# Kernel tuning notes

Hardware: AMD Instinct MI355X
Metric: run time of the kernel (lower is better)

Reference implementation:

```python
import jax, jax.numpy as jnp
import numpy as np

NUM_EXPERTS = 3
SCALING = 8.0 / 8.0  # alpha / r


def setup_inputs() -> dict:
    key = jax.random.key(0)
    ks = jax.random.split(key, 8)
    B, H, W, D = 64, 28, 28, 512
    Dh = 4 * D
    E, K, R = 3, 2, 8
    T = B * H * W
    x = jax.random.normal(ks[0], (B, H, W, D), dtype=jnp.float32)
    W1 = jax.random.normal(ks[1], (D, Dh), dtype=jnp.float32) * (1.0 / D ** 0.5)
    b1 = jnp.zeros((Dh,), dtype=jnp.float32)
    W2 = jax.random.normal(ks[2], (Dh, D), dtype=jnp.float32) * (1.0 / Dh ** 0.5)
    b2 = jnp.zeros((D,), dtype=jnp.float32)
    w_down = jax.random.normal(ks[3], (E, D, R), dtype=jnp.float32) * (1.0 / D ** 0.5)
    # original init is zeros; use small randn so output/grads are non-trivial
    w_up = jax.random.normal(ks[4], (E, R, D), dtype=jnp.float32) * 0.02
    gate_logits = jax.random.normal(ks[5], (T, E), dtype=jnp.float32)
    gate_probs = jax.nn.softmax(gate_logits, axis=-1)
    topk_probs, topk_indices = jax.lax.top_k(gate_probs, K)
    topk_indices = topk_indices.astype(jnp.int64)
    return {"x": x, "W1": W1, "b1": b1, "W2": W2, "b2": b2,
            "w_down": w_down, "w_up": w_up, "gate_probs": gate_probs,
            "topk_probs": topk_probs, "topk_indices": topk_indices}


def reference(x, W1, b1, W2, b2, w_down, w_up, gate_probs, topk_probs, topk_indices):
    # frozen base ConvNeXt MLP (channels-last): Linear -> GELU -> Linear
    orig_out = jax.nn.gelu(jnp.dot(x, W1) + b1, approximate=False) @ W2 + b2

    D = x.shape[-1]
    x_flat = x.reshape(-1, D)  # [T, D]

    # dense per-expert LoRA over all tokens (rank-8, cheap), then mask-combine
    down = jnp.einsum('td,edr->etr', x_flat, w_down)          # [E, T, r]
    up = jnp.einsum('etr,erd->etd', jax.nn.gelu(down, approximate=False), w_up) * SCALING  # [E, T, D]

    # weights[e, t] = sum_k topk_probs[t, k] * (topk_indices[t, k] == e)
    E = w_down.shape[0]
    mask = (topk_indices[None, :, :] == jnp.arange(E)[:, None, None])  # [E, T, K]
    weights = jnp.sum(jnp.where(mask, topk_probs[None], 0.0), axis=-1)  # [E, T]

    moe_out = jnp.einsum('et,etd->td', weights, up).reshape(x.shape)
    return orig_out + moe_out
```

## Files before the change

kernel.cpp:

```cpp
#include <hip/hip_runtime.h>

typedef _Float16 f16;
typedef _Float16 f16x8 __attribute__((ext_vector_type(8)));
typedef _Float16 f16x4 __attribute__((ext_vector_type(4)));
typedef float f32x4 __attribute__((ext_vector_type(4)));

#define TD 512
#define TDH 2048

__device__ __forceinline__ float gelu_fast(float x) {
  float u = x * fmaf(x * x, 0.0713548162f, 1.595769122f);
  float e = __expf(-u);
  return x * __builtin_amdgcn_rcpf(1.0f + e);
}

__device__ __forceinline__ void glds16(const f16* g, f16* l) {
  __builtin_amdgcn_global_load_lds(
      (const __attribute__((address_space(1))) void*)g,
      (__attribute__((address_space(3))) void*)l, 16, 0, 0);
}

__global__ __launch_bounds__(256) void k_conv_x(f16* __restrict__ dst,
                                                const float* __restrict__ src,
                                                int n4) {
  int i = blockIdx.x * 256 + threadIdx.x;
  if (i >= n4) return;
  float4 v = ((const float4*)src)[i];
  f16x4 o = {(f16)v.x, (f16)v.y, (f16)v.z, (f16)v.w};
  ((f16x4*)dst)[i] = o;
}

__global__ void k_trans(f16* __restrict__ dst, const float* __restrict__ src,
                        int R, int C) {
  __shared__ float t[32][33];
  const int bx = blockIdx.x, by = blockIdx.y;
  const int tx = threadIdx.x, ty = threadIdx.y;
#pragma unroll
  for (int s = 0; s < 32; s += 8)
    t[ty + s][tx] = src[(size_t)(by * 32 + ty + s) * C + bx * 32 + tx];
  __syncthreads();
#pragma unroll
  for (int s = 0; s < 32; s += 8)
    dst[(size_t)(bx * 32 + ty + s) * R + by * 32 + tx] = (f16)t[tx][ty + s];
}

__global__ __launch_bounds__(256) void k_wdT(f16* __restrict__ dst,
                                             const float* __restrict__ wd) {
  int i = blockIdx.x * 256 + threadIdx.x;
  int n = i >> 9, k = i & 511;
  float v = (n < 24) ? wd[(size_t)((n >> 3) * 512 + k) * 8 + (n & 7)] : 0.0f;
  dst[i] = (f16)v;
}

__global__ __launch_bounds__(256) void k_wuT(f16* __restrict__ dst,
                                             const float* __restrict__ wu) {
  int i = blockIdx.x * 256 + threadIdx.x;
  int d = i >> 5, er = i & 31;
  float v = (er < 24) ? wu[(size_t)(er >> 3) * 4096 + (er & 7) * 512 + d] : 0.0f;
  dst[i] = (f16)v;
}

template <int EPI, int NBN>
__global__ __launch_bounds__(256) void k_gemm(
    const f16* __restrict__ A, const f16* __restrict__ B, int Kt, int lda,
    int ldb, const float* __restrict__ bias, f16* __restrict__ Hout, int ldh,
    float* __restrict__ Out, int ldc, const float* __restrict__ tkp,
    const int* __restrict__ tki, const f16* __restrict__ Ag,
    const f16* __restrict__ Bg) {
  __shared__ __align__(16) f16 As[2][128 * 32];
  __shared__ __align__(16) f16 Bs[2][128 * 32];
  const int tid = threadIdx.x;
  const int lane = tid & 63;
  const int w = tid >> 6;
  const int wm = w >> 1, wn = w & 1;

  const int nwg = gridDim.x;
  const int q = nwg >> 3, r = nwg & 7;
  const int xcd = blockIdx.x & 7, pos = blockIdx.x >> 3;
  const int swz =
      (xcd < r ? xcd * (q + 1) : r * (q + 1) + (xcd - r) * q) + pos;
  const int bm = swz / NBN, bn = swz % NBN;

  const int c0 = 2 * w;
  const int lrow = lane >> 2;
  const int srow = c0 * 16 + lrow;
  const int skk = ((lane & 3) ^ ((lrow >> 1) & 3)) * 8;
  const f16* gA = A + (size_t)(bm * 128 + srow) * lda + skk;
  const f16* gB = B + (size_t)(bn * 128 + srow) * ldb + skk;
  f16* lA0 = &As[0][c0 * 512];
  f16* lA1 = &As[1][c0 * 512];
  f16* lB0 = &Bs[0][c0 * 512];
  f16* lB1 = &Bs[1][c0 * 512];

  f32x4 acc[4][4] = {};
  const int frow = lane & 15;
  const int swk = ((lane >> 4) ^ ((frow >> 1) & 3)) * 8;
  const int nt = Kt / 32;

  glds16(gA, lA0);
  glds16(gA + (size_t)16 * lda, lA0 + 512);
  glds16(gB, lB0);
  glds16(gB + (size_t)16 * ldb, lB0 + 512);
  __syncthreads();

  for (int t = 0; t < nt; ++t) {
    f16* dA = (t & 1) ? lA0 : lA1;
    f16* dB = (t & 1) ? lB0 : lB1;
    if (t + 1 < nt) {
      const int k = (t + 1) * 32;
      glds16(gA + k, dA);
      glds16(gA + k + (size_t)16 * lda, dA + 512);
      glds16(gB + k, dB);
      glds16(gB + k + (size_t)16 * ldb, dB + 512);
    } else if (EPI == 1) {
      const f16* gAg = Ag + (size_t)(bm * 128 + srow) * 32 + skk;
      const f16* gBg = Bg + (size_t)(bn * 128 + srow) * 32 + skk;
      glds16(gAg, dA);
      glds16(gAg + 512, dA + 512);
      glds16(gBg, dB);
      glds16(gBg + 512, dB + 512);
    }
    const f16* rA = As[t & 1];
    const f16* rB = Bs[t & 1];
    f16x8 af[4], bf[4];
#pragma unroll
    for (int i = 0; i < 4; i++)
      af[i] = *(const f16x8*)&rA[(wm * 64 + i * 16 + frow) * 32 + swk];
#pragma unroll
    for (int j = 0; j < 4; j++)
      bf[j] = *(const f16x8*)&rB[(wn * 64 + j * 16 + frow) * 32 + swk];
#pragma unroll
    for (int i = 0; i < 4; i++)
#pragma unroll
      for (int j = 0; j < 4; j++)
        acc[i][j] = __builtin_amdgcn_mfma_f32_16x16x32_f16(bf[j], af[i],
                                                           acc[i][j], 0, 0, 0);
    __syncthreads();
  }

  if constexpr (EPI == 1) {
    const f16* rA = As[nt & 1];
    const f16* rB = Bs[nt & 1];
    f16x8 af[4], bf[4];
#pragma unroll
    for (int i = 0; i < 4; i++)
      af[i] = *(const f16x8*)&rA[(wm * 64 + i * 16 + frow) * 32 + swk];
#pragma unroll
    for (int j = 0; j < 4; j++)
      bf[j] = *(const f16x8*)&rB[(wn * 64 + j * 16 + frow) * 32 + swk];
#pragma unroll
    for (int i = 0; i < 4; i++)
#pragma unroll
      for (int j = 0; j < 4; j++)
        acc[i][j] = __builtin_amdgcn_mfma_f32_16x16x32_f16(bf[j], af[i],
                                                           acc[i][j], 0, 0, 0);
  }

  const int m0 = wm * 64 + (lane & 15);
  const int n0 = wn * 64 + ((lane >> 4) << 2);

  if constexpr (EPI == 0) {
#pragma unroll
    for (int i = 0; i < 4; i++) {
      const size_t rb = (size_t)(bm * 128 + m0 + i * 16) * ldh + bn * 128 + n0;
#pragma unroll
      for (int j = 0; j < 4; j++) {
        const float4 bb = *(const float4*)&bias[bn * 128 + n0 + j * 16];
        f16x4 o = {(f16)gelu_fast(acc[i][j][0] + bb.x),
                   (f16)gelu_fast(acc[i][j][1] + bb.y),
                   (f16)gelu_fast(acc[i][j][2] + bb.z),
                   (f16)gelu_fast(acc[i][j][3] + bb.w)};
        *(f16x4*)&Hout[rb + j * 16] = o;
      }
    }
  } else if constexpr (EPI == 1) {
#pragma unroll
    for (int i = 0; i < 4; i++) {
      const size_t rb = (size_t)(bm * 128 + m0 + i * 16) * ldc + bn * 128 + n0;
#pragma unroll
      for (int j = 0; j < 4; j++) {
        const float4 bb = *(const float4*)&bias[bn * 128 + n0 + j * 16];
        float4 v = {acc[i][j][0] + bb.x, acc[i][j][1] + bb.y,
                    acc[i][j][2] + bb.z, acc[i][j][3] + bb.w};
        *(float4*)&Out[rb + j * 16] = v;
      }
    }
  } else {
    if (wn == 0) {
#pragma unroll
      for (int i = 0; i < 4; i++) {
        const int m = bm * 128 + m0 + i * 16;
        const int i0 = tki[m * 2], i1 = tki[m * 2 + 1];
        const float p0 = tkp[m * 2], p1 = tkp[m * 2 + 1];
#pragma unroll
        for (int j = 0; j < 2; j++) {
          const int nb = n0 + j * 16;
          const int e = nb >> 3;
          const float wgt = (i0 == e ? p0 : 0.0f) + (i1 == e ? p1 : 0.0f);
          f16x4 o = {(f16)(wgt * gelu_fast(acc[i][j][0])),
                     (f16)(wgt * gelu_fast(acc[i][j][1])),
                     (f16)(wgt * gelu_fast(acc[i][j][2])),
                     (f16)(wgt * gelu_fast(acc[i][j][3]))};
          *(f16x4*)&Hout[(size_t)m * 32 + nb] = o;
        }
      }
    }
  }
}

extern "C" void kernel_launch(void* const* d_in, const int* in_sizes, int n_in,
                              void* d_out, int out_size, void* d_ws,
                              size_t ws_size, hipStream_t stream) {
  const float* x = (const float*)d_in[0];
  const float* W1 = (const float*)d_in[1];
  const float* b1 = (const float*)d_in[2];
  const float* W2 = (const float*)d_in[3];
  const float* b2 = (const float*)d_in[4];
  const float* wd = (const float*)d_in[5];
  const float* wu = (const float*)d_in[6];
  const float* tkp = (const float*)d_in[8];
  const int* tki = (const int*)d_in[9];
  float* out = (float*)d_out;

  const int T = in_sizes[0] / TD;

  char* p = (char*)d_ws;
  f16* W1T = (f16*)p; p += (size_t)TDH * TD * sizeof(f16);
  f16* W2T = (f16*)p; p += (size_t)TD * TDH * sizeof(f16);
  f16* wdT = (f16*)p; p += (size_t)128 * TD * sizeof(f16);
  f16* wuT = (f16*)p; p += (size_t)TD * 32 * sizeof(f16);
  size_t fixed = (size_t)(p - (char*)d_ws);
  const size_t per_tok = (size_t)(TD + TDH + 32) * sizeof(f16);
  long mc = (long)((ws_size > fixed ? ws_size - fixed : 0) / per_tok);
  if (mc > T) mc = T;
  mc = (mc / 128) * 128;
  if (mc < 128) mc = 128;
  f16* xb = (f16*)p; p += (size_t)mc * TD * sizeof(f16);
  f16* Hb = (f16*)p; p += (size_t)mc * TDH * sizeof(f16);
  f16* gb = (f16*)p;

  k_trans<<<dim3(TDH / 32, TD / 32), dim3(32, 8), 0, stream>>>(W1T, W1, TD,
                                                               TDH);
  k_trans<<<dim3(TD / 32, TDH / 32), dim3(32, 8), 0, stream>>>(W2T, W2, TDH,
                                                               TD);
  k_wdT<<<dim3(65536 / 256), 256, 0, stream>>>(wdT, wd);
  k_wuT<<<dim3(16384 / 256), 256, 0, stream>>>(wuT, wu);

  for (long off = 0; off < T; off += mc) {
    long m = T - off;
    if (m > mc) m = mc;
    const int mt = (int)(m / 128);
    const int n4 = (int)(m * TD / 4);
    k_conv_x<<<dim3((n4 + 255) / 256), 256, 0, stream>>>(xb, x + off * TD, n4);
    k_gemm<2, 1><<<dim3(mt), 256, 0, stream>>>(
        xb, wdT, TD, TD, TD, nullptr, gb, 32, nullptr, 0, tkp + off * 2,
        tki + off * 2, nullptr, nullptr);
    k_gemm<0, 16><<<dim3(mt * 16), 256, 0, stream>>>(
        xb, W1T, TD, TD, TD, b1, Hb, TDH, nullptr, 0, nullptr, nullptr,
        nullptr, nullptr);
    k_gemm<1, 4><<<dim3(mt * 4), 256, 0, stream>>>(
        Hb, W2T, TDH, TDH, TDH, b2, nullptr, 0, out + off * TD, TD, nullptr,
        nullptr, gb, wuT);
  }
}
```

Before: 567.5 us.

## Widen GEMM K-tile to 64 and fold LoRA down-projection into first GEMM

The GEMM K-step doubles from 32 to 64 with a new XOR swizzle. That halves the number of barrier and loop iterations and issues two MFMAs per fragment pair. The LoRA down-projection is merged into the W1 GEMM as an extra 17th N-block, which removes a separate kernel launch and a second read of x. The gate buffer and up-weights are padded to 64 columns so the LoRA up-projection becomes one extra K-step in the W2 GEMM. The costs are double the LDS use (64KB), possible occupancy loss, and wasted MFMA work on the zero padding.

```diff
diff --git a/kernel.cpp b/kernel.cpp
--- a/kernel.cpp
+++ b/kernel.cpp
@@ -55,20 +55,20 @@
 __global__ __launch_bounds__(256) void k_wuT(f16* __restrict__ dst,
                                              const float* __restrict__ wu) {
   int i = blockIdx.x * 256 + threadIdx.x;
-  int d = i >> 5, er = i & 31;
+  int d = i >> 6, er = i & 63;
   float v = (er < 24) ? wu[(size_t)(er >> 3) * 4096 + (er & 7) * 512 + d] : 0.0f;
   dst[i] = (f16)v;
 }
 
 template <int EPI, int NBN>
-__global__ __launch_bounds__(256) void k_gemm(
-    const f16* __restrict__ A, const f16* __restrict__ B, int Kt, int lda,
-    int ldb, const float* __restrict__ bias, f16* __restrict__ Hout, int ldh,
-    float* __restrict__ Out, int ldc, const float* __restrict__ tkp,
-    const int* __restrict__ tki, const f16* __restrict__ Ag,
-    const f16* __restrict__ Bg) {
-  __shared__ __align__(16) f16 As[2][128 * 32];
-  __shared__ __align__(16) f16 Bs[2][128 * 32];
+__global__ __launch_bounds__(256) void k_gemm64(
+    const f16* __restrict__ A, const f16* __restrict__ B, int NT, int ntm,
+    int lda, int ldb, const float* __restrict__ bias, f16* __restrict__ Hout,
+    int ldh, f16* __restrict__ Gout, float* __restrict__ Out, int ldc,
+    const float* __restrict__ tkp, const int* __restrict__ tki,
+    const f16* __restrict__ Ag, const f16* __restrict__ Bg) {
+  __shared__ __align__(16) f16 As[2][128 * 64];
+  __shared__ __align__(16) f16 Bs[2][128 * 64];
   const int tid = threadIdx.x;
   const int lane = tid & 63;
   const int w = tid >> 6;
@@ -81,99 +81,124 @@
       (xcd < r ? xcd * (q + 1) : r * (q + 1) + (xcd - r) * q) + pos;
   const int bm = swz / NBN, bn = swz % NBN;
 
-  const int c0 = 2 * w;
-  const int lrow = lane >> 2;
-  const int srow = c0 * 16 + lrow;
-  const int skk = ((lane & 3) ^ ((lrow >> 1) & 3)) * 8;
-  const f16* gA = A + (size_t)(bm * 128 + srow) * lda + skk;
-  const f16* gB = B + (size_t)(bn * 128 + srow) * ldb + skk;
-  f16* lA0 = &As[0][c0 * 512];
-  f16* lA1 = &As[1][c0 * 512];
-  f16* lB0 = &Bs[0][c0 * 512];
-  f16* lB1 = &Bs[1][c0 * 512];
+  const int r0 = lane >> 3;
+  const int ssl = (lane & 7) ^ r0;
+  const f16* pA[4];
+  const f16* pB[4];
+  const f16* qA[4];
+  const f16* qB[4];
+#pragma unroll
+  for (int c = 0; c < 4; c++) {
+    const int rg = c * 4 + w;
+    const int row = rg * 8 + r0;
+    pA[c] = A + (size_t)(bm * 128 + row) * lda + ssl * 8;
+    pB[c] = B + (size_t)(bn * 128 + row) * ldb + ssl * 8;
+    if constexpr (EPI == 1) {
+      qA[c] = Ag + (size_t)(bm * 128 + row) * 64 + ssl * 8;
+      qB[c] = Bg + (size_t)(bn * 128 + row) * 64 + ssl * 8;
+    }
+  }
+
+#define STAGE(S, BUF)                                                    \
+  do {                                                                   \
+    if (EPI == 1 && (S) == ntm) {                                        \
+      _Pragma("unroll") for (int c = 0; c < 4; c++) {                    \
+        glds16(qA[c], &As[BUF][(c * 4 + w) * 512]);                      \
+        glds16(qB[c], &Bs[BUF][(c * 4 + w) * 512]);                      \
+      }                                                                  \
+    } else {                                                             \
+      const size_t o = (size_t)(S) * 64;                                 \
+      _Pragma("unroll") for (int c = 0; c < 4; c++) {                    \
+        glds16(pA[c] + o, &As[BUF][(c * 4 + w) * 512]);                  \
+        glds16(pB[c] + o, &Bs[BUF][(c * 4 + w) * 512]);                  \
+      }                                                                  \
+    }                                                                    \
+  } while (0)
 
   f32x4 acc[4][4] = {};
   const int frow = lane & 15;
-  const int swk = ((lane >> 4) ^ ((frow >> 1) & 3)) * 8;
-  const int nt = Kt / 32;
-
-  glds16(gA, lA0);
-  glds16(gA + (size_t)16 * lda, lA0 + 512);
-  glds16(gB, lB0);
-  glds16(gB + (size_t)16 * ldb, lB0 + 512);
+  const int fq = lane >> 4;
+  const int fx = frow & 7;
+  const int sA0 = ((fq ^ fx)) * 8;
+  const int sA1 = (((4 | fq) ^ fx)) * 8;
+  const int aRow = (wm * 64 + frow) * 64;
+  const int bRow = (wn * 64 + frow) * 64;
+
+  STAGE(0, 0);
   __syncthreads();
 
-  for (int t = 0; t < nt; ++t) {
-    f16* dA = (t & 1) ? lA0 : lA1;
-    f16* dB = (t & 1) ? lB0 : lB1;
-    if (t + 1 < nt) {
-      const int k = (t + 1) * 32;
-      glds16(gA + k, dA);
-      glds16(gA + k + (size_t)16 * lda, dA + 512);
-      glds16(gB + k, dB);
-      glds16(gB + k + (size_t)16 * ldb, dB + 512);
-    } else if (EPI == 1) {
-      const f16* gAg = Ag + (size_t)(bm * 128 + srow) * 32 + skk;
-      const f16* gBg = Bg + (size_t)(bn * 128 + srow) * 32 + skk;
-      glds16(gAg, dA);
-      glds16(gAg + 512, dA + 512);
-      glds16(gBg, dB);
-      glds16(gBg + 512, dB + 512);
-    }
+  for (int t = 0; t < NT; ++t) {
+    if (t + 1 < NT) STAGE(t + 1, (t + 1) & 1);
     const f16* rA = As[t & 1];
     const f16* rB = Bs[t & 1];
-    f16x8 af[4], bf[4];
+    f16x8 af[4][2], bf[4][2];
+#pragma unroll
+    for (int i = 0; i < 4; i++) {
+      af[i][0] = *(const f16x8*)&rA[aRow + i * 1024 + sA0];
+      af[i][1] = *(const f16x8*)&rA[aRow + i * 1024 + sA1];
+    }
+#pragma unroll
+    for (int j = 0; j < 4; j++) {
+      bf[j][0] = *(const f16x8*)&rB[bRow + j * 1024 + sA0];
+      bf[j][1] = *(const f16x8*)&rB[bRow + j * 1024 + sA1];
+    }
 #pragma unroll
     for (int i = 0; i < 4; i++)
-      af[i] = *(const f16x8*)&rA[(wm * 64 + i * 16 + frow) * 32 + swk];
-#pragma unroll
-    for (int j = 0; j < 4; j++)
-      bf[j] = *(const f16x8*)&rB[(wn * 64 + j * 16 + frow) * 32 + swk];
-#pragma unroll
-    for (int i = 0; i < 4; i++)
-#pragma unroll
-      for (int j = 0; j < 4; j++)
-        acc[i][j] = __builtin_amdgcn_mfma_f32_16x16x32_f16(bf[j], af[i],
+#pragma unroll
+      for (int j = 0; j < 4; j++) {
+        acc[i][j] = __builtin_amdgcn_mfma_f32_16x16x32_f16(bf[j][0], af[i][0],
                                                            acc[i][j], 0, 0, 0);
+        acc[i][j] = __builtin_amdgcn_mfma_f32_16x16x32_f16(bf[j][1], af[i][1],
+                                                           acc[i][j], 0, 0, 0);
+      }
     __syncthreads();
   }
-
-  if constexpr (EPI == 1) {
-    const f16* rA = As[nt & 1];
-    const f16* rB = Bs[nt & 1];
-    f16x8 af[4], bf[4];
-#pragma unroll
-    for (int i = 0; i < 4; i++)
-      af[i] = *(const f16x8*)&rA[(wm * 64 + i * 16 + frow) * 32 + swk];
-#pragma unroll
-    for (int j = 0; j < 4; j++)
-      bf[j] = *(const f16x8*)&rB[(wn * 64 + j * 16 + frow) * 32 + swk];
-#pragma unroll
-    for (int i = 0; i < 4; i++)
-#pragma unroll
-      for (int j = 0; j < 4; j++)
-        acc[i][j] = __builtin_amdgcn_mfma_f32_16x16x32_f16(bf[j], af[i],
-                                                           acc[i][j], 0, 0, 0);
-  }
-
-  const int m0 = wm * 64 + (lane & 15);
-  const int n0 = wn * 64 + ((lane >> 4) << 2);
+#undef STAGE
+
+  const int m0 = wm * 64 + frow;
+  const int n0 = wn * 64 + fq * 4;
 
   if constexpr (EPI == 0) {
-#pragma unroll
-    for (int i = 0; i < 4; i++) {
-      const size_t rb = (size_t)(bm * 128 + m0 + i * 16) * ldh + bn * 128 + n0;
-#pragma unroll
-      for (int j = 0; j < 4; j++) {
-        const float4 bb = *(const float4*)&bias[bn * 128 + n0 + j * 16];
-        f16x4 o = {(f16)gelu_fast(acc[i][j][0] + bb.x),
-                   (f16)gelu_fast(acc[i][j][1] + bb.y),
-                   (f16)gelu_fast(acc[i][j][2] + bb.z),
-                   (f16)gelu_fast(acc[i][j][3] + bb.w)};
-        *(f16x4*)&Hout[rb + j * 16] = o;
-      }
-    }
-  } else if constexpr (EPI == 1) {
+    if (bn != NBN - 1) {
+#pragma unroll
+      for (int i = 0; i < 4; i++) {
+        const size_t rb =
+            (size_t)(bm * 128 + m0 + i * 16) * ldh + bn * 128 + n0;
+#pragma unroll
+        for (int j = 0; j < 4; j++) {
+          const float4 bb = *(const float4*)&bias[bn * 128 + n0 + j * 16];
+          f16x4 o = {(f16)gelu_fast(acc[i][j][0] + bb.x),
+                     (f16)gelu_fast(acc[i][j][1] + bb.y),
+                     (f16)gelu_fast(acc[i][j][2] + bb.z),
+                     (f16)gelu_fast(acc[i][j][3] + bb.w)};
+          *(f16x4*)&Hout[rb + j * 16] = o;
+        }
+      }
+    } else if (wn == 0) {
+#pragma unroll
+      for (int i = 0; i < 4; i++) {
+        const int m = bm * 128 + m0 + i * 16;
+        const int i0 = tki[m * 2], i1 = tki[m * 2 + 1];
+        const float p0 = tkp[m * 2], p1 = tkp[m * 2 + 1];
+#pragma unroll
+        for (int j = 0; j < 4; j++) {
+          const int nb = n0 + j * 16;
+          f16x4 o;
+          if (j < 2) {
+            const int e = nb >> 3;
+            const float wgt = (i0 == e ? p0 : 0.0f) + (i1 == e ? p1 : 0.0f);
+            o = f16x4{(f16)(wgt * gelu_fast(acc[i][j][0])),
+                      (f16)(wgt * gelu_fast(acc[i][j][1])),
+                      (f16)(wgt * gelu_fast(acc[i][j][2])),
+                      (f16)(wgt * gelu_fast(acc[i][j][3]))};
+          } else {
+            o = f16x4{(f16)0.f, (f16)0.f, (f16)0.f, (f16)0.f};
+          }
+          *(f16x4*)&Gout[(size_t)m * 64 + nb] = o;
+        }
+      }
+    }
+  } else {
 #pragma unroll
     for (int i = 0; i < 4; i++) {
       const size_t rb = (size_t)(bm * 128 + m0 + i * 16) * ldc + bn * 128 + n0;
@@ -183,26 +208,6 @@
         float4 v = {acc[i][j][0] + bb.x, acc[i][j][1] + bb.y,
                     acc[i][j][2] + bb.z, acc[i][j][3] + bb.w};
         *(float4*)&Out[rb + j * 16] = v;
-      }
-    }
-  } else {
-    if (wn == 0) {
-#pragma unroll
-      for (int i = 0; i < 4; i++) {
-        const int m = bm * 128 + m0 + i * 16;
-        const int i0 = tki[m * 2], i1 = tki[m * 2 + 1];
-        const float p0 = tkp[m * 2], p1 = tkp[m * 2 + 1];
-#pragma unroll
-        for (int j = 0; j < 2; j++) {
-          const int nb = n0 + j * 16;
-          const int e = nb >> 3;
-          const float wgt = (i0 == e ? p0 : 0.0f) + (i1 == e ? p1 : 0.0f);
-          f16x4 o = {(f16)(wgt * gelu_fast(acc[i][j][0])),
-                     (f16)(wgt * gelu_fast(acc[i][j][1])),
-                     (f16)(wgt * gelu_fast(acc[i][j][2])),
-                     (f16)(wgt * gelu_fast(acc[i][j][3]))};
-          *(f16x4*)&Hout[(size_t)m * 32 + nb] = o;
-        }
       }
     }
   }
@@ -225,12 +230,11 @@
   const int T = in_sizes[0] / TD;
 
   char* p = (char*)d_ws;
-  f16* W1T = (f16*)p; p += (size_t)TDH * TD * sizeof(f16);
+  f16* W1Te = (f16*)p; p += (size_t)(TDH + 128) * TD * sizeof(f16);
   f16* W2T = (f16*)p; p += (size_t)TD * TDH * sizeof(f16);
-  f16* wdT = (f16*)p; p += (size_t)128 * TD * sizeof(f16);
-  f16* wuT = (f16*)p; p += (size_t)TD * 32 * sizeof(f16);
+  f16* wuT64 = (f16*)p; p += (size_t)TD * 64 * sizeof(f16);
   size_t fixed = (size_t)(p - (char*)d_ws);
-  const size_t per_tok = (size_t)(TD + TDH + 32) * sizeof(f16);
+  const size_t per_tok = (size_t)(TD + TDH + 64) * sizeof(f16);
   long mc = (long)((ws_size > fixed ? ws_size - fixed : 0) / per_tok);
   if (mc > T) mc = T;
   mc = (mc / 128) * 128;
@@ -239,12 +243,12 @@
   f16* Hb = (f16*)p; p += (size_t)mc * TDH * sizeof(f16);
   f16* gb = (f16*)p;
 
-  k_trans<<<dim3(TDH / 32, TD / 32), dim3(32, 8), 0, stream>>>(W1T, W1, TD,
+  k_trans<<<dim3(TDH / 32, TD / 32), dim3(32, 8), 0, stream>>>(W1Te, W1, TD,
                                                                TDH);
+  k_wdT<<<dim3(65536 / 256), 256, 0, stream>>>(W1Te + (size_t)TDH * TD, wd);
   k_trans<<<dim3(TD / 32, TDH / 32), dim3(32, 8), 0, stream>>>(W2T, W2, TDH,
                                                                TD);
-  k_wdT<<<dim3(65536 / 256), 256, 0, stream>>>(wdT, wd);
-  k_wuT<<<dim3(16384 / 256), 256, 0, stream>>>(wuT, wu);
+  k_wuT<<<dim3(32768 / 256), 256, 0, stream>>>(wuT64, wu);
 
   for (long off = 0; off < T; off += mc) {
     long m = T - off;
@@ -252,14 +256,11 @@
     const int mt = (int)(m / 128);
     const int n4 = (int)(m * TD / 4);
     k_conv_x<<<dim3((n4 + 255) / 256), 256, 0, stream>>>(xb, x + off * TD, n4);
-    k_gemm<2, 1><<<dim3(mt), 256, 0, stream>>>(
-        xb, wdT, TD, TD, TD, nullptr, gb, 32, nullptr, 0, tkp + off * 2,
-        tki + off * 2, nullptr, nullptr);
-    k_gemm<0, 16><<<dim3(mt * 16), 256, 0, stream>>>(
-        xb, W1T, TD, TD, TD, b1, Hb, TDH, nullptr, 0, nullptr, nullptr,
-        nullptr, nullptr);
-    k_gemm<1, 4><<<dim3(mt * 4), 256, 0, stream>>>(
-        Hb, W2T, TDH, TDH, TDH, b2, nullptr, 0, out + off * TD, TD, nullptr,
-        nullptr, gb, wuT);
-  }
-}
+    k_gemm64<0, 17><<<dim3(mt * 17), 256, 0, stream>>>(
+        xb, W1Te, TD / 64, TD / 64, TD, TD, b1, Hb, TDH, gb, nullptr, 0,
+        tkp + off * 2, tki + off * 2, nullptr, nullptr);
+    k_gemm64<1, 4><<<dim3(mt * 4), 256, 0, stream>>>(
+        Hb, W2T, TDH / 64 + 1, TDH / 64, TDH, TDH, b2, nullptr, 0, nullptr,
+        out + off * TD, TD, nullptr, nullptr, gb, wuT64);
+  }
+}
```

Result: slower. 588.5 us (+3.7%).
